# Performance work log

Measured on AMD Instinct MI355X. Metric: run time of the kernel, lower is better.

The kernel has to match this reference:

```python
import jax, jax.numpy as jnp
import numpy as np

N_USERS = 100000
N_ITEMS = 50000
EMB_DIM = 64
N_LAYERS = 2
N_INTENTS = 128
N_EDGES = 4000000
N_NODES = N_USERS + N_ITEMS


def setup_inputs() -> dict:
    key = jax.random.key(0)
    k1, k2, k3, k4, k5 = jax.random.split(key, 5)
    return {
        "user_emb": 0.1 * jax.random.normal(k1, (N_USERS, EMB_DIM), dtype=jnp.float32),
        "item_emb": 0.1 * jax.random.normal(k2, (N_ITEMS, EMB_DIM), dtype=jnp.float32),
        "intents": jax.random.normal(k3, (EMB_DIM, N_INTENTS), dtype=jnp.float32) * (2.0 / (EMB_DIM + N_INTENTS)) ** 0.5,
        "h_idx": jax.random.randint(k4, (N_EDGES,), 0, N_NODES, dtype=jnp.int64)
        if jax.config.jax_enable_x64 else jax.random.randint(k4, (N_EDGES,), 0, N_NODES, dtype=jnp.int32),
        "t_idx": jax.random.randint(k5, (N_EDGES,), 0, N_NODES, dtype=jnp.int32),
    }


def _spmm(h_idx, t_idx, g_vals, x):
    # y[h] += g_vals * x[t]  (sparse matrix @ dense, COO form)
    gathered = x[t_idx] * g_vals[:, None]  # [E, D]
    return jax.ops.segment_sum(gathered, h_idx, num_segments=N_NODES)


def reference(user_emb, item_emb, intents, h_idx, t_idx):
    # --- _cal_sparse_adj: G = D^{-1/2} A D^{-1/2}, A values are ones ---
    deg = jax.ops.segment_sum(jnp.ones_like(h_idx, dtype=user_emb.dtype), h_idx,
                              num_segments=N_NODES)
    d_inv_sqrt = jnp.where(deg > 0, jax.lax.rsqrt(jnp.maximum(deg, 1e-12)), 0.0)
    g_vals = d_inv_sqrt[h_idx] * d_inv_sqrt[t_idx]  # [E]

    # --- multi-layer propagation with intent-aware embeddings ---
    embs = jnp.concatenate([user_emb, item_emb], axis=0)  # [N, D]
    all_embs = [embs]
    for _ in range(N_LAYERS):
        gnn_embs = _spmm(h_idx, t_idx, g_vals, embs)  # [N, D]
        # intent projection: softmax over intents, reconstruct in emb space
        u, it = embs[:N_USERS], embs[N_USERS:]
        u_int = jax.nn.softmax(u @ intents, axis=1) @ intents.T      # [n_users, D]
        i_int = jax.nn.softmax(it @ intents, axis=1) @ intents.T     # [n_items, D]
        int_embs = jnp.concatenate([u_int, i_int], axis=0)
        embs = gnn_embs + int_embs
        all_embs.append(embs)
    out = jnp.sum(jnp.stack(all_embs, axis=1), axis=1) / len(all_embs)  # mean over layers
    return out
```

## Files before the change

kernel.cpp:

```cpp
#include <hip/hip_runtime.h>
#include <math.h>

#define N_USERS 100000
#define N_ITEMS 50000
#define N_NODES 150000
#define EMB 64
#define NI 128
#define NUM_EDGES 4000000
#define NPAD 150016
#define NB 586
#define BSTRIDE 8192
#define ETILE 8192
#define EGRID ((NUM_EDGES + ETILE - 1) / ETILE)
#define NT_ALL (NPAD / 16)
#define SBLK (NT_ALL / 4)
#define SENT 150000u

typedef __attribute__((ext_vector_type(8))) short bf16x8;
typedef __attribute__((ext_vector_type(4))) float f32x4;

__device__ __forceinline__ unsigned short f2bf(float f) {
    unsigned int u = __float_as_uint(f);
    u += 0x7FFFu + ((u >> 16) & 1u);
    return (unsigned short)(u >> 16);
}
__device__ __forceinline__ float bflo(unsigned int u) { return __uint_as_float(u << 16); }
__device__ __forceinline__ float bfhi(unsigned int u) { return __uint_as_float(u & 0xFFFF0000u); }


__global__ __launch_bounds__(512) void bucket_scatter(const int* __restrict__ h,
                                                      const int* __restrict__ t,
                                                      int* __restrict__ gcur,
                                                      unsigned int* __restrict__ ebuf) {
    __shared__ int lc[NB];
    __shared__ int lbase[NB];
    __shared__ int lcur[NB];
    int tid = threadIdx.x;
    for (int i = tid; i < NB; i += 512) lc[i] = 0;
    __syncthreads();
    int base = blockIdx.x * ETILE;
#pragma unroll
    for (int k = 0; k < ETILE / 512; ++k) {
        int idx = base + k * 512 + tid;
        if (idx < NUM_EDGES) atomicAdd(&lc[h[idx] >> 8], 1);
    }
    __syncthreads();
    for (int i = tid; i < NB; i += 512) {
        int c = lc[i];
        lbase[i] = c ? (i * BSTRIDE + atomicAdd(&gcur[i], c)) : 0;
        lcur[i] = 0;
    }
    __syncthreads();
#pragma unroll
    for (int k = 0; k < ETILE / 512; ++k) {
        int idx = base + k * 512 + tid;
        if (idx < NUM_EDGES) {
            int hh = h[idx], tt = t[idx];
            int b = hh >> 8;
            int p = lbase[b] + atomicAdd(&lcur[b], 1);
            int lim = b * BSTRIDE + BSTRIDE - 1;
            p = (p <= lim) ? p : lim;
            ebuf[p] = ((unsigned int)(hh & 255) << 18) | (unsigned int)tt;
        }
    }
}


__global__ __launch_bounds__(512) void bucket_csr(const int* __restrict__ gcur,
                                                  unsigned int* __restrict__ ebuf,
                                                  int2* __restrict__ rmeta,
                                                  float* __restrict__ dinv,
                                                  int* __restrict__ perm) {
    __shared__ unsigned int in_s[BSTRIDE];
    __shared__ int cnt_s[256];
    __shared__ int base_s[256];
    __shared__ int sc[256];
    __shared__ int dh[256];
    __shared__ int dcur[256];
    int b = blockIdx.x, tid = threadIdx.x;
    int s = b * BSTRIDE;
    int n = gcur[b];
    if (n > BSTRIDE) n = BSTRIDE;

    for (int i = tid; i < n; i += 512) in_s[i] = ebuf[s + i];
    if (tid < 256) { cnt_s[tid] = 0; dh[tid] = 0; dcur[tid] = 0; }
    __syncthreads();
    for (int i = tid; i < n; i += 512) atomicAdd(&cnt_s[in_s[i] >> 18], 1);
    __syncthreads();

    int c = 0, pc = 0, key = 0;
    if (tid < 256) {
        c = cnt_s[tid];
        pc = (c + 3) & ~3;
        sc[tid] = pc;
        key = 255 - min(c, 255);
        atomicAdd(&dh[key], 1);
    }
    __syncthreads();
    for (int off = 1; off < 256; off <<= 1) {
        int tv = 0;
        if (tid < 256 && tid >= off) tv = sc[tid - off];
        __syncthreads();
        if (tid < 256 && tid >= off) sc[tid] += tv;
        __syncthreads();
    }
    int excl = 0;
    if (tid < 256) { excl = sc[tid] - pc; base_s[tid] = excl; }
    __syncthreads();
    if (tid < 256) sc[tid] = dh[tid];
    __syncthreads();
    for (int off = 1; off < 256; off <<= 1) {
        int tv = 0;
        if (tid < 256 && tid >= off) tv = sc[tid - off];
        __syncthreads();
        if (tid < 256 && tid >= off) sc[tid] += tv;
        __syncthreads();
    }
    if (tid < 256) {
        int node = (b << 8) + tid;
        rmeta[node] = make_int2(s + excl, pc);
        dinv[node] = (c > 0) ? rsqrtf((float)c) : 0.0f;
        int pos = (sc[key] - dh[key]) + atomicAdd(&dcur[key], 1);
        perm[(b << 8) + pos] = node;
        for (int p2 = c; p2 < pc; ++p2) ebuf[s + excl + p2] = SENT;
        cnt_s[tid] = 0;
    }
    __syncthreads();
    for (int i = tid; i < n; i += 512) {
        unsigned int qv = in_s[i];
        int hl = (int)(qv >> 18);
        int p = base_s[hl] + atomicAdd(&cnt_s[hl], 1);
        ebuf[s + p] = qv & 0x3FFFFu;
    }
}


__global__ void init_kernel(const float4* __restrict__ ue4, const float4* __restrict__ ie4,
                            uint2* __restrict__ ebf4, float4* __restrict__ out4) {
    int i = blockIdx.x * blockDim.x + threadIdx.x;
    const int uelems = N_USERS * EMB / 4;
    const int relems = N_NODES * EMB / 4;
    const int total  = NPAD * EMB / 4;
    if (i < total) {
        float4 v = make_float4(0.f, 0.f, 0.f, 0.f);
        if (i < uelems) v = ue4[i];
        else if (i < relems) v = ie4[i - uelems];
        if (i < relems) out4[i] = v;
        unsigned int p0 = ((unsigned int)f2bf(v.y) << 16) | f2bf(v.x);
        unsigned int p1 = ((unsigned int)f2bf(v.w) << 16) | f2bf(v.z);
        ebf4[i] = make_uint2(p0, p1);
    }
}


__global__ __launch_bounds__(256) void wconv(const float* __restrict__ W,
                                             unsigned short* __restrict__ Wt,
                                             unsigned short* __restrict__ W2b) {
    int i = blockIdx.x * 256 + threadIdx.x;
    if (i < EMB * NI) {
        int d = i >> 7, c = i & 127;
        unsigned short b = f2bf(W[i]);
        W2b[i] = b;
        Wt[c * EMB + d] = b;
    }
}


__global__ __launch_bounds__(256, 7) void spmm_intent(const int2* __restrict__ rmeta,
                                                      const unsigned int* __restrict__ col,
                                                      const float* __restrict__ dinv,
                                                      const int* __restrict__ perm,
                                                      const unsigned short* __restrict__ ebf,
                                                      unsigned short* __restrict__ ebfout,
                                                      const unsigned short* __restrict__ Wt,
                                                      const unsigned short* __restrict__ W2b,
                                                      float* __restrict__ acc, float scale) {
    __shared__ __align__(16) float UPool[4][1408];

    int tid = threadIdx.x;
    int wid = tid >> 6, lane = tid & 63;
    int q = lane >> 4, c = lane & 15;
    int qq = lane >> 3, cc = lane & 7;
    int tile = blockIdx.x * 4 + wid;
    if (tile >= NT_ALL) return;
    int rowbase = tile << 4;
    float* fw = &UPool[wid][0];
    unsigned short* pw = (unsigned short*)&UPool[wid][1088];

#pragma unroll 1
    for (int half = 0; half < 2; ++half) {
        int prow = perm[rowbase + half * 8 + qq];
        int2 rm = rmeta[prow];
        int s = rm.x, pcv = rm.y;
        float dr = dinv[prow];

        float a0 = 0.f, a1 = 0.f, a2 = 0.f, a3 = 0.f;
        float a4 = 0.f, a5 = 0.f, a6 = 0.f, a7 = 0.f;
        const unsigned short* eb = ebf + (cc << 3);

        int e0 = (int)(col[s]     & 0x3FFFFu);
        int e1 = (int)(col[s + 1] & 0x3FFFFu);
        int e2 = (int)(col[s + 2] & 0x3FFFFu);
        int e3 = (int)(col[s + 3] & 0x3FFFFu);
        float g0 = dinv[e0], g1 = dinv[e1], g2 = dinv[e2], g3 = dinv[e3];
        uint4 u0 = *(const uint4*)(eb + ((size_t)e0 << 6));
        uint4 u1 = *(const uint4*)(eb + ((size_t)e1 << 6));
        uint4 u2 = *(const uint4*)(eb + ((size_t)e2 << 6));
        uint4 u3 = *(const uint4*)(eb + ((size_t)e3 << 6));
        int f0 = (int)(col[s + 4] & 0x3FFFFu);
        int f1 = (int)(col[s + 5] & 0x3FFFFu);
        int f2 = (int)(col[s + 6] & 0x3FFFFu);
        int f3 = (int)(col[s + 7] & 0x3FFFFu);

        for (int it = 0; it < pcv; it += 4) {
            float h0 = dinv[f0], h1 = dinv[f1], h2 = dinv[f2], h3 = dinv[f3];
            uint4 v0 = *(const uint4*)(eb + ((size_t)f0 << 6));
            uint4 v1 = *(const uint4*)(eb + ((size_t)f1 << 6));
            uint4 v2 = *(const uint4*)(eb + ((size_t)f2 << 6));
            uint4 v3 = *(const uint4*)(eb + ((size_t)f3 << 6));
            int x0 = (int)(col[s + it + 8]  & 0x3FFFFu);
            int x1 = (int)(col[s + it + 9]  & 0x3FFFFu);
            int x2 = (int)(col[s + it + 10] & 0x3FFFFu);
            int x3 = (int)(col[s + it + 11] & 0x3FFFFu);
            a0 = fmaf(g0, bflo(u0.x), a0); a1 = fmaf(g0, bfhi(u0.x), a1);
            a2 = fmaf(g0, bflo(u0.y), a2); a3 = fmaf(g0, bfhi(u0.y), a3);
            a4 = fmaf(g0, bflo(u0.z), a4); a5 = fmaf(g0, bfhi(u0.z), a5);
            a6 = fmaf(g0, bflo(u0.w), a6); a7 = fmaf(g0, bfhi(u0.w), a7);
            a0 = fmaf(g1, bflo(u1.x), a0); a1 = fmaf(g1, bfhi(u1.x), a1);
            a2 = fmaf(g1, bflo(u1.y), a2); a3 = fmaf(g1, bfhi(u1.y), a3);
            a4 = fmaf(g1, bflo(u1.z), a4); a5 = fmaf(g1, bfhi(u1.z), a5);
            a6 = fmaf(g1, bflo(u1.w), a6); a7 = fmaf(g1, bfhi(u1.w), a7);
            a0 = fmaf(g2, bflo(u2.x), a0); a1 = fmaf(g2, bfhi(u2.x), a1);
            a2 = fmaf(g2, bflo(u2.y), a2); a3 = fmaf(g2, bfhi(u2.y), a3);
            a4 = fmaf(g2, bflo(u2.z), a4); a5 = fmaf(g2, bfhi(u2.z), a5);
            a6 = fmaf(g2, bflo(u2.w), a6); a7 = fmaf(g2, bfhi(u2.w), a7);
            a0 = fmaf(g3, bflo(u3.x), a0); a1 = fmaf(g3, bfhi(u3.x), a1);
            a2 = fmaf(g3, bflo(u3.y), a2); a3 = fmaf(g3, bfhi(u3.y), a3);
            a4 = fmaf(g3, bflo(u3.z), a4); a5 = fmaf(g3, bfhi(u3.z), a5);
            a6 = fmaf(g3, bflo(u3.w), a6); a7 = fmaf(g3, bfhi(u3.w), a7);
            u0 = v0; u1 = v1; u2 = v2; u3 = v3;
            g0 = h0; g1 = h1; g2 = h2; g3 = h3;
            f0 = x0; f1 = x1; f2 = x2; f3 = x3;
        }
        int fb = (half * 8 + qq) * 68 + (cc << 3);
        fw[fb + 0] = a0 * dr; fw[fb + 1] = a1 * dr;
        fw[fb + 2] = a2 * dr; fw[fb + 3] = a3 * dr;
        fw[fb + 4] = a4 * dr; fw[fb + 5] = a5 * dr;
        fw[fb + 6] = a6 * dr; fw[fb + 7] = a7 * dr;
    }

    int arow = perm[rowbase + c];
    const unsigned short* erow = ebf + ((size_t)arow << 6);
    bf16x8 A0 = *(const bf16x8*)(erow + (q << 3));
    bf16x8 A1 = *(const bf16x8*)(erow + 32 + (q << 3));
    f32x4 S[8];
#pragma unroll
    for (int t = 0; t < 8; ++t) {
        bf16x8 B0 = *(const bf16x8*)&Wt[(16 * t + c) * EMB + (q << 3)];
        bf16x8 B1 = *(const bf16x8*)&Wt[(16 * t + c) * EMB + 32 + (q << 3)];
        f32x4 z = {0.f, 0.f, 0.f, 0.f};
        z = __builtin_amdgcn_mfma_f32_16x16x32_bf16(A0, B0, z, 0, 0, 0);
        S[t] = __builtin_amdgcn_mfma_f32_16x16x32_bf16(A1, B1, z, 0, 0, 0);
    }

#pragma unroll
    for (int r = 0; r < 4; ++r) {
        float m = S[0][r];
#pragma unroll
        for (int t = 1; t < 8; ++t) m = fmaxf(m, S[t][r]);
        m = fmaxf(m, __shfl_xor(m, 1)); m = fmaxf(m, __shfl_xor(m, 2));
        m = fmaxf(m, __shfl_xor(m, 4)); m = fmaxf(m, __shfl_xor(m, 8));
        float sum = 0.f;
#pragma unroll
        for (int t = 0; t < 8; ++t) { float ex = __expf(S[t][r] - m); S[t][r] = ex; sum += ex; }
        sum += __shfl_xor(sum, 1); sum += __shfl_xor(sum, 2);
        sum += __shfl_xor(sum, 4); sum += __shfl_xor(sum, 8);
        float inv = 1.0f / sum;
#pragma unroll
        for (int t = 0; t < 8; ++t) S[t][r] *= inv;
    }

    f32x4 O0 = {0.f, 0.f, 0.f, 0.f}, O1 = O0, O2 = O0, O3 = O0;
#pragma unroll
    for (int s2 = 0; s2 < 4; ++s2) {
#pragma unroll
        for (int h2 = 0; h2 < 2; ++h2) {
            int t = 2 * s2 + h2;
#pragma unroll
            for (int r = 0; r < 4; ++r) {
                float p = S[t][r];
                unsigned short b = f2bf(p);
                pw[(4 * q + r) * 40 + (h2 << 4) + c] = b;
                S[t][r] = p - bflo((unsigned int)b);
            }
        }
        bf16x8 Pf = *(const bf16x8*)&pw[c * 40 + (q << 3)];
        {
            bf16x8 Bf0 = *(const bf16x8*)&W2b[(c) * NI + (s2 << 5) + (q << 3)];
            bf16x8 Bf1 = *(const bf16x8*)&W2b[(16 + c) * NI + (s2 << 5) + (q << 3)];
            O0 = __builtin_amdgcn_mfma_f32_16x16x32_bf16(Pf, Bf0, O0, 0, 0, 0);
            O1 = __builtin_amdgcn_mfma_f32_16x16x32_bf16(Pf, Bf1, O1, 0, 0, 0);
            bf16x8 Bf2 = *(const bf16x8*)&W2b[(32 + c) * NI + (s2 << 5) + (q << 3)];
            bf16x8 Bf3 = *(const bf16x8*)&W2b[(48 + c) * NI + (s2 << 5) + (q << 3)];
            O2 = __builtin_amdgcn_mfma_f32_16x16x32_bf16(Pf, Bf2, O2, 0, 0, 0);
            O3 = __builtin_amdgcn_mfma_f32_16x16x32_bf16(Pf, Bf3, O3, 0, 0, 0);
        }
#pragma unroll
        for (int h2 = 0; h2 < 2; ++h2) {
            int t = 2 * s2 + h2;
#pragma unroll
            for (int r = 0; r < 4; ++r)
                pw[(4 * q + r) * 40 + (h2 << 4) + c] = f2bf(S[t][r]);
        }
        bf16x8 Pl = *(const bf16x8*)&pw[c * 40 + (q << 3)];
        {
            bf16x8 Bf0 = *(const bf16x8*)&W2b[(c) * NI + (s2 << 5) + (q << 3)];
            bf16x8 Bf1 = *(const bf16x8*)&W2b[(16 + c) * NI + (s2 << 5) + (q << 3)];
            O0 = __builtin_amdgcn_mfma_f32_16x16x32_bf16(Pl, Bf0, O0, 0, 0, 0);
            O1 = __builtin_amdgcn_mfma_f32_16x16x32_bf16(Pl, Bf1, O1, 0, 0, 0);
            bf16x8 Bf2 = *(const bf16x8*)&W2b[(32 + c) * NI + (s2 << 5) + (q << 3)];
            bf16x8 Bf3 = *(const bf16x8*)&W2b[(48 + c) * NI + (s2 << 5) + (q << 3)];
            O2 = __builtin_amdgcn_mfma_f32_16x16x32_bf16(Pl, Bf2, O2, 0, 0, 0);
            O3 = __builtin_amdgcn_mfma_f32_16x16x32_bf16(Pl, Bf3, O3, 0, 0, 0);
        }
    }

    asm volatile("" ::: "memory");

#pragma unroll
    for (int r = 0; r < 4; ++r) {
        int rl = 4 * q + r;
        float* gr = &fw[rl * 68];
        gr[c]      += O0[r];
        gr[16 + c] += O1[r];
        gr[32 + c] += O2[r];
        gr[48 + c] += O3[r];
    }

    {
        int j = lane >> 2, sg = lane & 3;
        int rw = perm[rowbase + j];
        const float* gr = &fw[j * 68 + (sg << 4)];
        float4 x0 = *(const float4*)&gr[0];
        float4 x1 = *(const float4*)&gr[4];
        float4 x2 = *(const float4*)&gr[8];
        float4 x3 = *(const float4*)&gr[12];
        size_t base = ((size_t)rw << 6) + (sg << 4);
        uint4 w0, w1;
        w0.x = (unsigned int)f2bf(x0.x) | ((unsigned int)f2bf(x0.y) << 16);
        w0.y = (unsigned int)f2bf(x0.z) | ((unsigned int)f2bf(x0.w) << 16);
        w0.z = (unsigned int)f2bf(x1.x) | ((unsigned int)f2bf(x1.y) << 16);
        w0.w = (unsigned int)f2bf(x1.z) | ((unsigned int)f2bf(x1.w) << 16);
        w1.x = (unsigned int)f2bf(x2.x) | ((unsigned int)f2bf(x2.y) << 16);
        w1.y = (unsigned int)f2bf(x2.z) | ((unsigned int)f2bf(x2.w) << 16);
        w1.z = (unsigned int)f2bf(x3.x) | ((unsigned int)f2bf(x3.y) << 16);
        w1.w = (unsigned int)f2bf(x3.z) | ((unsigned int)f2bf(x3.w) << 16);
        *(uint4*)(ebfout + base) = w0;
        *(uint4*)(ebfout + base + 8) = w1;
        if (rw < N_NODES) {
            float4* ap = (float4*)(acc + base);
            float4 b0 = ap[0], b1 = ap[1], b2 = ap[2], b3 = ap[3];
            b0.x = (b0.x + x0.x) * scale; b0.y = (b0.y + x0.y) * scale;
            b0.z = (b0.z + x0.z) * scale; b0.w = (b0.w + x0.w) * scale;
            b1.x = (b1.x + x1.x) * scale; b1.y = (b1.y + x1.y) * scale;
            b1.z = (b1.z + x1.z) * scale; b1.w = (b1.w + x1.w) * scale;
            b2.x = (b2.x + x2.x) * scale; b2.y = (b2.y + x2.y) * scale;
            b2.z = (b2.z + x2.z) * scale; b2.w = (b2.w + x2.w) * scale;
            b3.x = (b3.x + x3.x) * scale; b3.y = (b3.y + x3.y) * scale;
            b3.z = (b3.z + x3.z) * scale; b3.w = (b3.w + x3.w) * scale;
            ap[0] = b0; ap[1] = b1; ap[2] = b2; ap[3] = b3;
        }
    }
}


extern "C" void kernel_launch(void* const* d_in, const int* in_sizes, int n_in,
                              void* d_out, int out_size, void* d_ws, size_t ws_size,
                              hipStream_t stream) {
    const float* ue = (const float*)d_in[0];
    const float* ie = (const float*)d_in[1];
    const float* W  = (const float*)d_in[2];
    const int*   h  = (const int*)d_in[3];
    const int*   t  = (const int*)d_in[4];
    float* out = (float*)d_out;

    int*            gcur  = (int*)d_ws;
    int2*           rmeta = (int2*)(gcur + 1024);
    float*          dinv  = (float*)(rmeta + NPAD);
    int*            perm  = (int*)(dinv + NPAD);
    unsigned short* ebfA  = (unsigned short*)(perm + NPAD);
    unsigned short* ebfB  = ebfA + (size_t)NPAD * EMB;
    unsigned int*   ebuf  = (unsigned int*)(ebfB + (size_t)NPAD * EMB);
    unsigned short* Wt    = (unsigned short*)(ebuf + NB * BSTRIDE + 16);
    unsigned short* W2b   = Wt + EMB * NI;

    hipMemsetAsync(gcur, 0, NB * sizeof(int), stream);
    hipMemsetAsync(ebuf + NB * BSTRIDE, 0, 16 * sizeof(unsigned int), stream);
    bucket_scatter<<<EGRID, 512, 0, stream>>>(h, t, gcur, ebuf);
    bucket_csr<<<NB, 512, 0, stream>>>(gcur, ebuf, rmeta, dinv, perm);
    init_kernel<<<(NPAD * EMB / 4 + 255) / 256, 256, 0, stream>>>(
        (const float4*)ue, (const float4*)ie, (uint2*)ebfA, (float4*)out);
    wconv<<<(EMB * NI + 255) / 256, 256, 0, stream>>>(W, Wt, W2b);

    const unsigned int* col = ebuf;
    spmm_intent<<<SBLK, 256, 0, stream>>>(rmeta, col, dinv, perm, ebfA, ebfB, Wt, W2b, out, 1.0f);
    spmm_intent<<<SBLK, 256, 0, stream>>>(rmeta, col, dinv, perm, ebfB, ebfA, Wt, W2b, out, 1.0f / 3.0f);
}
```

Measured before the change: 488.0 us.

## Halve CSR bucket size and sort rows by degree within 16-row groups

Buckets now cover 128 destination nodes instead of 256, doubling the bucket count and shrinking per-bucket shared buffers. The histogram-based degree sort across 256 rows is replaced by a local rank within each group of 16 rows, which removes a second prefix-scan pass. This is meant to cut bucket_csr cost and raise block-level parallelism. The catch is a weaker load-balance ordering for the SpMM and a smaller per-bucket capacity of 4352, which leaves less headroom for degree skew before edges get clamped.

```diff
diff --git a/kernel.cpp b/kernel.cpp
--- a/kernel.cpp
+++ b/kernel.cpp
@@ -8,8 +8,8 @@
 #define NI 128
 #define NUM_EDGES 4000000
 #define NPAD 150016
-#define NB 586
-#define BSTRIDE 8192
+#define NB 1172
+#define BSTRIDE 4352
 #define ETILE 8192
 #define EGRID ((NUM_EDGES + ETILE - 1) / ETILE)
 #define NT_ALL (NPAD / 16)
@@ -42,7 +42,7 @@
 #pragma unroll
     for (int k = 0; k < ETILE / 512; ++k) {
         int idx = base + k * 512 + tid;
-        if (idx < NUM_EDGES) atomicAdd(&lc[h[idx] >> 8], 1);
+        if (idx < NUM_EDGES) atomicAdd(&lc[h[idx] >> 7], 1);
     }
     __syncthreads();
     for (int i = tid; i < NB; i += 512) {
@@ -56,11 +56,11 @@
         int idx = base + k * 512 + tid;
         if (idx < NUM_EDGES) {
             int hh = h[idx], tt = t[idx];
-            int b = hh >> 8;
+            int b = hh >> 7;
             int p = lbase[b] + atomicAdd(&lcur[b], 1);
             int lim = b * BSTRIDE + BSTRIDE - 1;
             p = (p <= lim) ? p : lim;
-            ebuf[p] = ((unsigned int)(hh & 255) << 18) | (unsigned int)tt;
+            ebuf[p] = ((unsigned int)(hh & 127) << 18) | (unsigned int)tt;
         }
     }
 }
@@ -72,56 +72,50 @@
                                                   float* __restrict__ dinv,
                                                   int* __restrict__ perm) {
     __shared__ unsigned int in_s[BSTRIDE];
-    __shared__ int cnt_s[256];
-    __shared__ int base_s[256];
-    __shared__ int sc[256];
-    __shared__ int dh[256];
-    __shared__ int dcur[256];
+    __shared__ int cnt_s[128];
+    __shared__ int base_s[128];
+    __shared__ int sc[128];
+    __shared__ int dg[128];
     int b = blockIdx.x, tid = threadIdx.x;
     int s = b * BSTRIDE;
     int n = gcur[b];
     if (n > BSTRIDE) n = BSTRIDE;
 
     for (int i = tid; i < n; i += 512) in_s[i] = ebuf[s + i];
-    if (tid < 256) { cnt_s[tid] = 0; dh[tid] = 0; dcur[tid] = 0; }
+    if (tid < 128) cnt_s[tid] = 0;
     __syncthreads();
     for (int i = tid; i < n; i += 512) atomicAdd(&cnt_s[in_s[i] >> 18], 1);
     __syncthreads();
 
-    int c = 0, pc = 0, key = 0;
-    if (tid < 256) {
+    int c = 0, pc = 0;
+    if (tid < 128) {
         c = cnt_s[tid];
         pc = (c + 3) & ~3;
         sc[tid] = pc;
-        key = 255 - min(c, 255);
-        atomicAdd(&dh[key], 1);
-    }
-    __syncthreads();
-    for (int off = 1; off < 256; off <<= 1) {
+        dg[tid] = c;
+    }
+    __syncthreads();
+    for (int off = 1; off < 128; off <<= 1) {
         int tv = 0;
-        if (tid < 256 && tid >= off) tv = sc[tid - off];
+        if (tid < 128 && tid >= off) tv = sc[tid - off];
         __syncthreads();
-        if (tid < 256 && tid >= off) sc[tid] += tv;
+        if (tid < 128 && tid >= off) sc[tid] += tv;
         __syncthreads();
     }
-    int excl = 0;
-    if (tid < 256) { excl = sc[tid] - pc; base_s[tid] = excl; }
-    __syncthreads();
-    if (tid < 256) sc[tid] = dh[tid];
-    __syncthreads();
-    for (int off = 1; off < 256; off <<= 1) {
-        int tv = 0;
-        if (tid < 256 && tid >= off) tv = sc[tid - off];
-        __syncthreads();
-        if (tid < 256 && tid >= off) sc[tid] += tv;
-        __syncthreads();
-    }
-    if (tid < 256) {
-        int node = (b << 8) + tid;
+    if (tid < 128) {
+        int excl = sc[tid] - pc;
+        base_s[tid] = excl;
+        int node = (b << 7) + tid;
         rmeta[node] = make_int2(s + excl, pc);
         dinv[node] = (c > 0) ? rsqrtf((float)c) : 0.0f;
-        int pos = (sc[key] - dh[key]) + atomicAdd(&dcur[key], 1);
-        perm[(b << 8) + pos] = node;
+        int tb = tid & ~15;
+        int rank = 0;
+#pragma unroll
+        for (int j = 0; j < 16; ++j) {
+            int dj = dg[tb + j];
+            rank += (dj > c) || (dj == c && (tb + j) < tid);
+        }
+        perm[(b << 7) + tb + rank] = node;
         for (int p2 = c; p2 < pc; ++p2) ebuf[s + excl + p2] = SENT;
         cnt_s[tid] = 0;
     }
@@ -385,7 +379,7 @@
     float* out = (float*)d_out;
 
     int*            gcur  = (int*)d_ws;
-    int2*           rmeta = (int2*)(gcur + 1024);
+    int2*           rmeta = (int2*)(gcur + 2048);
     float*          dinv  = (float*)(rmeta + NPAD);
     int*            perm  = (int*)(dinv + NPAD);
     unsigned short* ebfA  = (unsigned short*)(perm + NPAD);
```

Measured after the change: 473.2 us. -3.0%, faster.
